# Kernel tuning notes

Hardware: AMD Instinct MI355X
Metric: run time of the kernel (lower is better)

The kernel has to match this reference:

```python
import jax, jax.numpy as jnp
import numpy as np

B, L, D, ORDER, POS, HID, LMAX = 4, 4096, 1024, 2, 65, 64, 4096
K2 = (POS - 1) // 2

def _layernorm(x, w, b, eps=1e-5):
    m = jnp.mean(x, -1, keepdims=True)
    v = jnp.mean((x - m) ** 2, -1, keepdims=True)
    return (x - m) * jax.lax.rsqrt(v + eps) * w + b

def _fftconv(x, h, d):
    # torch: rfft(h, 2L, norm='forward') * rfft(x, 2L) -> irfft(.., norm='forward')
    # net scaling equals standard (unnormalized fwd / 1-over-n inverse) circular conv,
    # which is exactly jnp.fft default conventions.
    n = 2 * x.shape[-1]
    y = jnp.fft.irfft(jnp.fft.rfft(x, n=n) * jnp.fft.rfft(h, n=n), n=n)[..., : x.shape[-1]]
    return y + x * d

def setup_inputs() -> dict:
    key = jax.random.key(0)
    ks = jax.random.split(key, 12)
    s = 0.05
    # PositionalEncoding buffers/params (deterministic init, as in torch __init__)
    t = np.linspace(0, 1, LMAX, dtype=np.float64)[:, None]
    t_pos = np.arange(LMAX, dtype=np.float64)[:, None]
    k = np.arange(K2, dtype=np.float64)[None, :]
    z = np.exp(1j * 2 * np.pi * k * t_pos / LMAX)
    pos_z = np.concatenate([t, z.real, z.imag], axis=-1).astype(np.float32)  # (LMAX, POS)
    pos_t = t.reshape(1, 1, LMAX).astype(np.float32)
    # ExponentialDecayWindow alphas (deterministic init)
    max_decay = np.log(0.01) / 0.3
    min_decay = np.log(0.01) / 1.5
    alphas = np.linspace(min_decay, max_decay, D).reshape(1, D, 1).astype(np.float32)
    H3 = (ORDER + 1) * D
    return dict(
        u=jax.random.normal(ks[0], (B, L, D), jnp.float32),
        norm1_w=jnp.ones((D,), jnp.float32), norm1_b=jnp.zeros((D,), jnp.float32),
        proj_w=jax.random.normal(ks[1], (H3, D), jnp.float32) * s,
        proj_b=jnp.zeros((H3,), jnp.float32),
        conv_w=jax.random.normal(ks[2], (H3, 1, 3), jnp.float32) * 0.3,
        conv_b=jnp.zeros((H3,), jnp.float32),
        pos_t=jnp.asarray(pos_t), pos_z=jnp.asarray(pos_z),
        fnn_w0=jax.random.normal(ks[3], (HID, POS), jnp.float32) * s,
        fnn_b0=jnp.zeros((HID,), jnp.float32),
        freq0=8.0 * jnp.ones((1, HID), jnp.float32),
        fnn_w1=jax.random.normal(ks[4], (HID, HID), jnp.float32) * s,
        fnn_b1=jnp.zeros((HID,), jnp.float32),
        freq1=8.0 * jnp.ones((1, HID), jnp.float32),
        fnn_w2=jax.random.normal(ks[5], (HID, HID), jnp.float32) * s,
        fnn_b2=jnp.zeros((HID,), jnp.float32),
        freq2=8.0 * jnp.ones((1, HID), jnp.float32),
        fnn_wout=jax.random.normal(ks[6], (ORDER * D, HID), jnp.float32) * s,
        alphas=jnp.asarray(alphas),
        hy_bias=jax.random.normal(ks[7], (ORDER, 1, D, 1), jnp.float32),
        norm2_w=jnp.ones((D,), jnp.float32), norm2_b=jnp.zeros((D,), jnp.float32),
        fc_w=jax.random.normal(ks[8], (D, D), jnp.float32) * s,
        fc_b=jnp.zeros((D,), jnp.float32),
    )

def reference(u, norm1_w, norm1_b, proj_w, proj_b, conv_w, conv_b, pos_t, pos_z,
              fnn_w0, fnn_b0, freq0, fnn_w1, fnn_b1, freq1, fnn_w2, fnn_b2, freq2,
              fnn_wout, alphas, hy_bias, norm2_w, norm2_b, fc_w, fc_b):
    Lq = u.shape[1]
    # Projection: LN -> Linear -> depthwise short conv (causal-ish, pad=2, slice :L)
    x = _layernorm(u, norm1_w, norm1_b)
    x = jnp.einsum('bld,hd->blh', x, proj_w) + proj_b          # (B,L,3D)
    x = x.transpose(0, 2, 1)                                   # (B,3D,L)
    x = jax.lax.conv_general_dilated(
        x, conv_w, window_strides=(1,), padding=[(2, 2)],
        feature_group_count=x.shape[1],
        dimension_numbers=('NCH', 'OIH', 'NCH'))[..., :Lq] + conv_b[None, :, None]
    # HyenaFilter: sin-MLP over positional features, then exp-decay window
    zf = pos_z[:Lq]                                            # (L,POS)
    h = jnp.sin(freq0 * (zf @ fnn_w0.T + fnn_b0))
    h = jnp.sin(freq1 * (h @ fnn_w1.T + fnn_b1))
    h = jnp.sin(freq2 * (h @ fnn_w2.T + fnn_b2))
    h = (h @ fnn_wout.T).T.reshape(ORDER, D, Lq)               # (order,D,L)
    decay = jnp.exp(alphas * pos_t[..., :Lq])                  # (1,D,L)
    h = h * decay
    # order-wise gated FFT long convolution (faithful to torch chunk/broadcast semantics)
    v = x[:, -1:, :]                                           # (B,1,L)
    for i in range(ORDER):
        v = x[:, i:i + 1, :] * _fftconv(v, h[i][None], hy_bias[i])  # (B,D,L)
    y = u + v.transpose(0, 2, 1)
    out = _layernorm(y, norm2_w, norm2_b) @ fc_w.T + fc_b      # activation = identity
    return out + y
```

## Files before the change

### kernel.cpp

```cpp
#include <hip/hip_runtime.h>
#include <hip/hip_bf16.h>

#define LL 4096
#define DD 1024
#define NB 4
#define N4 4096
#define KBINS 4097
#define NSLOT4 4366
#define PI_F 3.14159265358979323846f
#define INV4 (1.0f / 4096.0f)

typedef __attribute__((ext_vector_type(4))) float f32x4;
typedef __attribute__((ext_vector_type(8))) short s16x8;

#if defined(__has_builtin)
#if __has_builtin(__builtin_amdgcn_global_load_lds)
#define USE_GLOAD_LDS 1
#endif
#endif
#ifndef USE_GLOAD_LDS
#define USE_GLOAD_LDS 0
#endif

__device__ __forceinline__ unsigned short f2bf(float f) {
  unsigned int x = __float_as_uint(f);
  x += 0x7fffu + ((x >> 16) & 1u);
  return (unsigned short)(x >> 16);
}

__device__ __forceinline__ int SLT(int n) { return n + (n >> 4) + (n >> 8); }
__device__ __forceinline__ int brev12(int n) { return (int)(__brev((unsigned)n) >> 20); }

__device__ __forceinline__ float2 cmul(float2 a, float2 b) {
  return make_float2(a.x * b.x - a.y * b.y, a.x * b.y + a.y * b.x);
}
__device__ __forceinline__ float2 cadd(float2 a, float2 b) { return make_float2(a.x + b.x, a.y + b.y); }
__device__ __forceinline__ float2 csub(float2 a, float2 b) { return make_float2(a.x - b.x, a.y - b.y); }
__device__ __forceinline__ float2 conjf(float2 a) { return make_float2(a.x, -a.y); }
__device__ __forceinline__ float2 mulni(float2 v) { return make_float2(v.y, -v.x); }
__device__ __forceinline__ float2 mulpi(float2 v) { return make_float2(-v.y, v.x); }

template<bool INV>
__device__ __forceinline__ void bfly8(float2& A0, float2& A1, float2& A2, float2& A3,
                                      float2& A4, float2& A5, float2& A6, float2& A7,
                                      float2 w1, float2 w2, float2 w3) {
  const float C8 = 0.70710678118654752f;
  float2 t;
  t = cmul(w1, A1); float2 b0 = cadd(A0, t), b1 = csub(A0, t);
  t = cmul(w1, A3); float2 b2 = cadd(A2, t), b3 = csub(A2, t);
  t = cmul(w1, A5); float2 b4 = cadd(A4, t), b5 = csub(A4, t);
  t = cmul(w1, A7); float2 b6 = cadd(A6, t), b7 = csub(A6, t);
  t = cmul(w2, b2);                     float2 c0 = cadd(b0, t), c2 = csub(b0, t);
  t = cmul(w2, b3); t = INV ? mulpi(t) : mulni(t);
  float2 c1 = cadd(b1, t), c3 = csub(b1, t);
  t = cmul(w2, b6);                     float2 c4 = cadd(b4, t), c6 = csub(b4, t);
  t = cmul(w2, b7); t = INV ? mulpi(t) : mulni(t);
  float2 c5 = cadd(b5, t), c7 = csub(b5, t);
  t = cmul(w3, c4); A0 = cadd(c0, t); A4 = csub(c0, t);
  float2 e1 = cmul(w3, c5);
  t = INV ? make_float2(C8 * (e1.x - e1.y), C8 * (e1.y + e1.x))
          : make_float2(C8 * (e1.x + e1.y), C8 * (e1.y - e1.x));
  A1 = cadd(c1, t); A5 = csub(c1, t);
  float2 e2 = cmul(w3, c6); t = INV ? mulpi(e2) : mulni(e2);
  A2 = cadd(c2, t); A6 = csub(c2, t);
  float2 e3 = cmul(w3, c7);
  t = INV ? make_float2(-C8 * (e3.x + e3.y), C8 * (e3.x - e3.y))
          : make_float2(C8 * (e3.y - e3.x), -C8 * (e3.x + e3.y));
  A3 = cadd(c3, t); A7 = csub(c3, t);
}

template<bool INV>
__device__ __forceinline__ void fft4k_01(float2* Z, const float2* __restrict__ tw) {
  const int tid = threadIdx.x;
#pragma unroll
  for (int p = 0; p < 3; ++p) {
    const int hs = 3 * p;
    const int h = 1 << hs;
    const int j0 = tid & (h - 1);
    const int i = ((tid >> hs) << (hs + 3)) + j0;
    int s0 = SLT(i),         s1 = SLT(i + h),     s2 = SLT(i + 2 * h), s3 = SLT(i + 3 * h);
    int s4 = SLT(i + 4 * h), s5 = SLT(i + 5 * h), s6 = SLT(i + 6 * h), s7 = SLT(i + 7 * h);
    float2 a0 = Z[s0], a1 = Z[s1], a2 = Z[s2], a3 = Z[s3];
    float2 a4 = Z[s4], a5 = Z[s5], a6 = Z[s6], a7 = Z[s7];
    float2 w1 = tw[j0 << (12 - hs)];
    float2 w2 = tw[j0 << (11 - hs)];
    float2 w3 = tw[j0 << (10 - hs)];
    if (INV) { w1.y = -w1.y; w2.y = -w2.y; w3.y = -w3.y; }
    bfly8<INV>(a0, a1, a2, a3, a4, a5, a6, a7, w1, w2, w3);
    Z[s0] = a0; Z[s1] = a1; Z[s2] = a2; Z[s3] = a3;
    Z[s4] = a4; Z[s5] = a5; Z[s6] = a6; Z[s7] = a7;
    __builtin_amdgcn_wave_barrier();
  }
}

template<bool INV>
__device__ __forceinline__ void fft4k_p3(const float2* Z, const float2* __restrict__ tw,
                                         float2 d[8]) {
  const int t = threadIdx.x;
#pragma unroll
  for (int k = 0; k < 8; ++k) d[k] = Z[SLT(t + 512 * k)];
  float2 w1 = tw[t << 3], w2 = tw[t << 2], w3 = tw[t << 1];
  if (INV) { w1.y = -w1.y; w2.y = -w2.y; w3.y = -w3.y; }
  bfly8<INV>(d[0], d[1], d[2], d[3], d[4], d[5], d[6], d[7], w1, w2, w3);
}

__global__ void k_prep(float2* tw, const float* __restrict__ fcw,
                       unsigned short* __restrict__ fcwb) {
  const int bid = blockIdx.x;
  if (bid < 16) {
    int k = bid * 256 + threadIdx.x;
    float ang = -2.0f * PI_F * (float)k / 8192.0f;
    float s, c;
    sincosf(ang, &s, &c);
    tw[k] = make_float2(c, s);
  } else {
    int i = (bid - 16) * 256 + threadIdx.x;
    float4 v = ((const float4*)fcw)[i];
    ushort4 o;
    o.x = f2bf(v.x); o.y = f2bf(v.y); o.z = f2bf(v.z); o.w = f2bf(v.w);
    ((ushort4*)fcwb)[i] = o;
  }
}

__global__ __launch_bounds__(256) void k_lnproj_ffn(
    const float* __restrict__ u, const float* __restrict__ n1w, const float* __restrict__ n1b,
    const float* __restrict__ pw, const float* __restrict__ pb,
    float* __restrict__ xp0, float* __restrict__ xp1, float* __restrict__ xpL,
    const float* __restrict__ pos_z,
    const float* __restrict__ w0, const float* __restrict__ b0, const float* __restrict__ f0,
    const float* __restrict__ w1, const float* __restrict__ b1, const float* __restrict__ f1,
    const float* __restrict__ w2, const float* __restrict__ b2, const float* __restrict__ f2,
    float* __restrict__ hid2T) {
  __shared__ float zin[4][66];
  __shared__ float hbuf[4][64];
  const int g = threadIdx.x >> 6, lane = threadIdx.x & 63;
  if (blockIdx.x < (NB * LL) / 4) {
    const int r = blockIdx.x * 4 + g;
    const float* ur = u + (size_t)r * DD;
    float4 uv[4];
    float s = 0.f, sq = 0.f;
#pragma unroll
    for (int c = 0; c < 4; ++c) {
      uv[c] = ((const float4*)ur)[lane + 64 * c];
      s += uv[c].x + uv[c].y + uv[c].z + uv[c].w;
      sq += uv[c].x * uv[c].x + uv[c].y * uv[c].y + uv[c].z * uv[c].z + uv[c].w * uv[c].w;
    }
    for (int m = 1; m < 64; m <<= 1) { s += __shfl_xor(s, m); sq += __shfl_xor(sq, m); }
    const float mean = s * (1.0f / DD);
    const float var = sq * (1.0f / DD) - mean * mean;
    const float rs = rsqrtf(var + 1e-5f);
    float d0 = 0.f, d1 = 0.f, dL = 0.f;
    const float* pwL = pw + (size_t)3071 * DD;
#pragma unroll
    for (int c = 0; c < 4; ++c) {
      int i4 = lane + 64 * c;
      float4 wv = ((const float4*)n1w)[i4];
      float4 bv = ((const float4*)n1b)[i4];
      float4 p0 = ((const float4*)pw)[i4];
      float4 p1v = ((const float4*)(pw + DD))[i4];
      float4 pLv = ((const float4*)pwL)[i4];
      float xn;
      xn = (uv[c].x - mean) * rs * wv.x + bv.x; d0 += xn * p0.x; d1 += xn * p1v.x; dL += xn * pLv.x;
      xn = (uv[c].y - mean) * rs * wv.y + bv.y; d0 += xn * p0.y; d1 += xn * p1v.y; dL += xn * pLv.y;
      xn = (uv[c].z - mean) * rs * wv.z + bv.z; d0 += xn * p0.z; d1 += xn * p1v.z; dL += xn * pLv.z;
      xn = (uv[c].w - mean) * rs * wv.w + bv.w; d0 += xn * p0.w; d1 += xn * p1v.w; dL += xn * pLv.w;
    }
    for (int m = 1; m < 64; m <<= 1) {
      d0 += __shfl_xor(d0, m); d1 += __shfl_xor(d1, m); dL += __shfl_xor(dL, m);
    }
    if (lane == 0) {
      xp0[r] = d0 + pb[0];
      xp1[r] = d1 + pb[1];
      xpL[r] = dL + pb[3071];
    }
  } else {
    const int l0 = (blockIdx.x - (NB * LL) / 4) * 16;
    for (int it = 0; it < 4; ++it) {
      const int l = l0 + g * 4 + it;
      zin[g][lane] = pos_z[(size_t)l * 65 + lane];
      if (lane == 0) zin[g][64] = pos_z[(size_t)l * 65 + 64];
      __syncthreads();
      float acc = b0[lane];
#pragma unroll
      for (int k = 0; k < 65; ++k) acc += zin[g][k] * w0[lane * 65 + k];
      float hv = sinf(f0[lane] * acc);
      __syncthreads();
      hbuf[g][lane] = hv;
      __syncthreads();
      acc = b1[lane];
#pragma unroll
      for (int k = 0; k < 64; ++k) acc += hbuf[g][k] * w1[lane * 64 + k];
      hv = sinf(f1[lane] * acc);
      __syncthreads();
      hbuf[g][lane] = hv;
      __syncthreads();
      acc = b2[lane];
#pragma unroll
      for (int k = 0; k < 64; ++k) acc += hbuf[g][k] * w2[lane * 64 + k];
      hv = sinf(f2[lane] * acc);
      hid2T[(size_t)lane * LL + l] = hv;
      __syncthreads();
    }
  }
}

__global__ __launch_bounds__(256) void k_tapconv(
    const float* __restrict__ xp0, const float* __restrict__ xp1, const float* __restrict__ xpL,
    const float* __restrict__ cw, const float* __restrict__ cb,
    float* __restrict__ x0c, float* __restrict__ x1c, float* __restrict__ xLc) {
  int idx = blockIdx.x * 256 + threadIdx.x;
  if (idx >= NB * LL) return;
  int l = idx & (LL - 1);
  int base = idx - l;
  {
    const float* a = xp0 + base;
    float v = cw[2] * a[l];
    if (l >= 1) v += cw[1] * a[l - 1];
    if (l >= 2) v += cw[0] * a[l - 2];
    x0c[idx] = v + cb[0];
  }
  {
    const float* a = xp1 + base;
    float v = cw[5] * a[l];
    if (l >= 1) v += cw[4] * a[l - 1];
    if (l >= 2) v += cw[3] * a[l - 2];
    x1c[idx] = v + cb[1];
  }
  {
    const float* a = xpL + base;
    float v = cw[3071 * 3 + 2] * a[l];
    if (l >= 1) v += cw[3071 * 3 + 1] * a[l - 1];
    if (l >= 2) v += cw[3071 * 3 + 0] * a[l - 2];
    xLc[idx] = v + cb[3071];
  }
}

#define FG_CH 16
__global__ __launch_bounds__(256) void k_filter_gemm(
    const float* __restrict__ hid2T, const float* __restrict__ wout,
    const float* __restrict__ alphas, const float* __restrict__ pos_t,
    float* __restrict__ h) {
  __shared__ float wdl[FG_CH][64];
  const int cg = blockIdx.x & 127;
  const int lg = blockIdx.x >> 7;
  const int t = threadIdx.x;
  for (int idx = t; idx < FG_CH * 64; idx += 256) {
    int c = idx >> 6, k = idx & 63;
    wdl[c][k] = wout[(size_t)(cg * FG_CH + c) * 64 + k];
  }
  __syncthreads();
  const int l0 = lg * 1024 + 4 * t;
  float4 acc[FG_CH];
#pragma unroll
  for (int c = 0; c < FG_CH; ++c) acc[c] = make_float4(0.f, 0.f, 0.f, 0.f);
  for (int k = 0; k < 64; ++k) {
    float4 hv = *(const float4*)&hid2T[(size_t)k * LL + l0];
#pragma unroll
    for (int c = 0; c < FG_CH; ++c) {
      acc[c].x = fmaf(hv.x, wdl[c][k], acc[c].x);
      acc[c].y = fmaf(hv.y, wdl[c][k], acc[c].y);
      acc[c].z = fmaf(hv.z, wdl[c][k], acc[c].z);
      acc[c].w = fmaf(hv.w, wdl[c][k], acc[c].w);
    }
  }
  float4 tt = *(const float4*)&pos_t[l0];
#pragma unroll
  for (int c = 0; c < FG_CH; ++c) {
    int ch = cg * FG_CH + c;
    float a = alphas[ch & (DD - 1)];
    float4 o;
    o.x = acc[c].x * expf(a * tt.x);
    o.y = acc[c].y * expf(a * tt.y);
    o.z = acc[c].z * expf(a * tt.z);
    o.w = acc[c].w * expf(a * tt.w);
    *(float4*)&h[(size_t)ch * LL + l0] = o;
  }
}

__global__ __launch_bounds__(512, 4) void k_fft_filters(
    const float* __restrict__ h, const float* __restrict__ xLc,
    float2* __restrict__ Hs, float2* __restrict__ V0s, const float2* __restrict__ tw) {
  __shared__ float2 Z[NSLOT4];
  const int tid = threadIdx.x;
  const int bid = blockIdx.x;
  const float2* src = (bid < 2048) ? (const float2*)(h + (size_t)bid * LL)
                                   : (const float2*)(xLc + (size_t)(bid - 2048) * LL);
  float2* Out = (bid < 2048) ? (Hs + (size_t)bid * KBINS)
                             : (V0s + (size_t)(bid - 2048) * KBINS);
#pragma unroll
  for (int gi = 0; gi < 4; ++gi) {
    int j = tid + gi * 512;
    float2 v = src[j];
    int r = brev12(j);
    Z[SLT(r)] = v;
    Z[SLT(r + 1)] = make_float2(0.f, 0.f);
  }
  __syncthreads();
  fft4k_01<false>(Z, tw);
  __syncthreads();
  float2 dd[8];
  fft4k_p3<false>(Z, tw, dd);
#pragma unroll
  for (int k = 0; k < 8; ++k) Z[SLT(tid + 512 * k)] = dd[k];
  __syncthreads();
#pragma unroll
  for (int gi = 0; gi < 4; ++gi) {
    int k = tid + gi * 512;
    float2 zk = Z[SLT(k)];
    float2 zm = Z[SLT((N4 - k) & (N4 - 1))];
    float2 B = conjf(zm);
    float2 E = make_float2(0.5f * (zk.x + B.x), 0.5f * (zk.y + B.y));
    float2 F = make_float2(0.5f * (zk.x - B.x), 0.5f * (zk.y - B.y));
    float2 G = cmul(tw[k], F);
    float2 WO = mulni(G);
    Out[k] = cadd(E, WO);
    Out[N4 - k] = conjf(csub(E, WO));
  }
  if (tid == 0) {
    float2 zc = Z[SLT(2048)];
    float2 F = make_float2(0.f, zc.y);
    float2 G = cmul(tw[2048], F);
    Out[2048] = cadd(make_float2(zc.x, 0.f), mulni(G));
  }
}

__global__ __launch_bounds__(512, 4) void k_conv12(
    const float2* __restrict__ Hs, const float2* __restrict__ V0s,
    const float* __restrict__ x0c, const float* __restrict__ x1c, const float* __restrict__ xLc,
    const float* __restrict__ hyb, float* __restrict__ v2, const float2* __restrict__ tw) {
  __shared__ float2 Z[NSLOT4];
  const int b = blockIdx.x >> 10, d = blockIdx.x & 1023;
  const int tid = threadIdx.x;
  const float2* H0 = Hs + (size_t)d * KBINS;
  const float2* H1 = Hs + (size_t)(DD + d) * KBINS;
  const float2* V = V0s + (size_t)b * KBINS;
  const float2* g0 = (const float2*)(x0c + (size_t)b * LL);
  const float2* g1 = (const float2*)(x1c + (size_t)b * LL);
  const float2* v0 = (const float2*)(xLc + (size_t)b * LL);
  float2 gg0[4], vv0[4];
#pragma unroll
  for (int k = 0; k < 4; ++k) {
    int j = tid + 512 * k;
    gg0[k] = g0[j];
    vv0[k] = v0[j];
  }
#pragma unroll
  for (int gi = 0; gi < 4; ++gi) {
    int k = tid + gi * 512;
    int m = N4 - k;
    float2 Yk = cmul(V[k], H0[k]);
    float2 Ym = cmul(V[m], H0[m]);
    float2 B = conjf(Ym);
    float2 E = make_float2(0.5f * (Yk.x + B.x), 0.5f * (Yk.y + B.y));
    float2 F = make_float2(0.5f * (Yk.x - B.x), 0.5f * (Yk.y - B.y));
    float2 O = cmul(conjf(tw[k]), F);
    float2 iO = mulpi(O);
    Z[SLT(brev12(k))] = cadd(E, iO);
    if (k > 0) Z[SLT(brev12(m))] = conjf(csub(E, iO));
  }
  if (tid == 0) {
    float2 A = cmul(V[2048], H0[2048]);
    float2 F = make_float2(0.f, A.y);
    float2 O = cmul(conjf(tw[2048]), F);
    Z[SLT(brev12(2048))] = cadd(make_float2(A.x, 0.f), mulpi(O));
  }
  __syncthreads();
  fft4k_01<true>(Z, tw);
  __syncthreads();
  float2 dA[8];
  fft4k_p3<true>(Z, tw, dA);
  const float bd0 = hyb[d], bd1 = hyb[DD + d];
  float2 vsave[4];
#pragma unroll
  for (int k = 0; k < 4; ++k) {
    vsave[k] = make_float2(gg0[k].x * fmaf(dA[k].x, INV4, bd0 * vv0[k].x),
                           gg0[k].y * fmaf(dA[k].y, INV4, bd0 * vv0[k].y));
  }
  __syncthreads();
#pragma unroll
  for (int k = 0; k < 4; ++k) {
    int j = tid + 512 * k;
    int r = brev12(j);
    Z[SLT(r)] = vsave[k];
    Z[SLT(r + 1)] = make_float2(0.f, 0.f);
  }
  __syncthreads();
  fft4k_01<false>(Z, tw);
  __syncthreads();
  float2 dB[8];
  fft4k_p3<false>(Z, tw, dB);
#pragma unroll
  for (int k = 0; k < 8; ++k) Z[SLT(tid + 512 * k)] = dB[k];
  __syncthreads();
  float2 gg1[4];
#pragma unroll
  for (int k = 0; k < 4; ++k) gg1[k] = g1[tid + 512 * k];
  float2 zpk[4], zpm[4], z2048;
#pragma unroll
  for (int gi = 0; gi < 4; ++gi) {
    int k = tid + gi * 512;
    int m = N4 - k;
    float2 zk = Z[SLT(k)];
    float2 zm = Z[SLT(m & (N4 - 1))];
    float2 B = conjf(zm);
    float2 E = make_float2(0.5f * (zk.x + B.x), 0.5f * (zk.y + B.y));
    float2 F = make_float2(0.5f * (zk.x - B.x), 0.5f * (zk.y - B.y));
    float2 wk = tw[k];
    float2 G = cmul(wk, F);
    float2 WO = mulni(G);
    float2 Xk = cadd(E, WO);
    float2 Xm = conjf(csub(E, WO));
    float2 Yk = cmul(Xk, H1[k]);
    float2 Ym = cmul(Xm, H1[m]);
    float2 B2 = conjf(Ym);
    float2 E2 = make_float2(0.5f * (Yk.x + B2.x), 0.5f * (Yk.y + B2.y));
    float2 F2 = make_float2(0.5f * (Yk.x - B2.x), 0.5f * (Yk.y - B2.y));
    float2 O2 = cmul(conjf(wk), F2);
    float2 iO2 = mulpi(O2);
    zpk[gi] = cadd(E2, iO2);
    zpm[gi] = conjf(csub(E2, iO2));
  }
  if (tid == 0) {
    float2 zc = Z[SLT(2048)];
    float2 F = make_float2(0.f, zc.y);
    float2 G = cmul(tw[2048], F);
    float2 Xk = cadd(make_float2(zc.x, 0.f), mulni(G));
    float2 Y = cmul(Xk, H1[2048]);
    float2 F2 = make_float2(0.f, Y.y);
    float2 O2 = cmul(conjf(tw[2048]), F2);
    z2048 = cadd(make_float2(Y.x, 0.f), mulpi(O2));
  }
  __syncthreads();
#pragma unroll
  for (int gi = 0; gi < 4; ++gi) {
    int k = tid + gi * 512;
    Z[SLT(brev12(k))] = zpk[gi];
    if (k > 0) Z[SLT(brev12(N4 - k))] = zpm[gi];
  }
  if (tid == 0) Z[SLT(brev12(2048))] = z2048;
  __syncthreads();
  fft4k_01<true>(Z, tw);
  __syncthreads();
  float2 dC[8];
  fft4k_p3<true>(Z, tw, dC);
  float2* out2 = (float2*)(v2 + ((size_t)b * DD + d) * LL);
#pragma unroll
  for (int k = 0; k < 4; ++k) {
    int j = tid + 512 * k;
    out2[j] = make_float2(gg1[k].x * fmaf(dC[k].x, INV4, bd1 * vsave[k].x),
                          gg1[k].y * fmaf(dC[k].y, INV4, bd1 * vsave[k].y));
  }
}

__global__ __launch_bounds__(256) void k_transpose_add(const float* __restrict__ v2,
                                                       const float* __restrict__ u,
                                                       float* __restrict__ y) {
  __shared__ float T[64][65];
  const int bid = blockIdx.x;
  const int lt = bid & 63, dt = (bid >> 6) & 15, b = bid >> 10;
  const int t = threadIdx.x;
  const int tdr = t >> 2, lc0 = (t & 3) * 16;
  const float* vp = v2 + ((size_t)(b * DD + dt * 64 + tdr)) * LL + lt * 64 + lc0;
#pragma unroll
  for (int q = 0; q < 4; ++q) {
    float4 vv = ((const float4*)vp)[q];
    T[tdr][lc0 + 4 * q + 0] = vv.x;
    T[tdr][lc0 + 4 * q + 1] = vv.y;
    T[tdr][lc0 + 4 * q + 2] = vv.z;
    T[tdr][lc0 + 4 * q + 3] = vv.w;
  }
  __syncthreads();
  const int dc = t & 63, lg = t >> 6;
#pragma unroll
  for (int lr0 = 0; lr0 < 64; lr0 += 4) {
    int lr = lr0 + lg;
    size_t idx = ((size_t)b * LL + lt * 64 + lr) * DD + dt * 64 + dc;
    y[idx] = u[idx] + T[dc][lr];
  }
}

__global__ __launch_bounds__(256) void k_ln2(const float* __restrict__ y,
                                             const float* __restrict__ w,
                                             const float* __restrict__ bb,
                                             unsigned short* __restrict__ yln) {
  const int wid = threadIdx.x >> 6, lane = threadIdx.x & 63;
  const size_t r = (size_t)blockIdx.x * 4 + wid;
  const float* yr = y + r * DD;
  float4 v[4];
  float s = 0.f, sq = 0.f;
#pragma unroll
  for (int c = 0; c < 4; ++c) {
    v[c] = ((const float4*)yr)[lane + 64 * c];
    s += v[c].x + v[c].y + v[c].z + v[c].w;
    sq += v[c].x * v[c].x + v[c].y * v[c].y + v[c].z * v[c].z + v[c].w * v[c].w;
  }
  for (int m = 1; m < 64; m <<= 1) { s += __shfl_xor(s, m); sq += __shfl_xor(sq, m); }
  const float mean = s * (1.0f / DD);
  const float var = sq * (1.0f / DD) - mean * mean;
  const float rs = rsqrtf(var + 1e-5f);
#pragma unroll
  for (int c = 0; c < 4; ++c) {
    int i4 = lane + 64 * c;
    float4 wv = ((const float4*)w)[i4];
    float4 bv = ((const float4*)bb)[i4];
    ushort4 o;
    o.x = f2bf((v[c].x - mean) * rs * wv.x + bv.x);
    o.y = f2bf((v[c].y - mean) * rs * wv.y + bv.y);
    o.z = f2bf((v[c].z - mean) * rs * wv.z + bv.z);
    o.w = f2bf((v[c].w - mean) * rs * wv.w + bv.w);
    ((ushort4*)(yln + r * DD))[i4] = o;
  }
}

#define GBM 128
#define GBN 128
#define GBK 64
#if USE_GLOAD_LDS
#define LDK 64
#else
#define LDK 72
#endif

__global__ __launch_bounds__(256) void k_gemm(const short* __restrict__ A,
                                              const short* __restrict__ Bw,
                                              const float* __restrict__ fcb,
                                              const float* __restrict__ yy,
                                              float* __restrict__ out) {
  __shared__ short As[GBM * LDK];
  __shared__ short Bs[GBN * LDK];
  const int t = threadIdx.x;
  const int bm = blockIdx.x & 127;
  const int bn = blockIdx.x >> 7;
  const int wave = t >> 6, lane = t & 63;
  const int wr = wave >> 1, wc = wave & 1;
  const int rrow = lane & 15, kb = (lane >> 4) * 8;

  f32x4 acc[4][4];
#pragma unroll
  for (int i = 0; i < 4; ++i)
#pragma unroll
    for (int j = 0; j < 4; ++j) acc[i][j] = (f32x4){0.f, 0.f, 0.f, 0.f};

  const size_t abase = (size_t)(bm * GBM) * 1024;
  const size_t bbase = (size_t)(bn * GBN) * 1024;

  for (int k0 = 0; k0 < 1024; k0 += GBK) {
#if USE_GLOAD_LDS
    {
      const int r0 = wave * 32;
      const int lrow = lane >> 3, loff = (lane & 7) * 8;
#pragma unroll
      for (int q = 0; q < 4; ++q) {
        const int row = r0 + 8 * q + lrow;
        __builtin_amdgcn_global_load_lds(
            (const __attribute__((address_space(1))) void*)(A + abase + (size_t)row * 1024 + k0 + loff),
            (__attribute__((address_space(3))) void*)&As[(r0 + 8 * q) * LDK], 16, 0, 0);
        __builtin_amdgcn_global_load_lds(
            (const __attribute__((address_space(1))) void*)(Bw + bbase + (size_t)row * 1024 + k0 + loff),
            (__attribute__((address_space(3))) void*)&Bs[(r0 + 8 * q) * LDK], 16, 0, 0);
      }
    }
#else
#pragma unroll
    for (int c = 0; c < 4; ++c) {
      int chunk = c * 256 + t;
      int row = chunk >> 3, off = (chunk & 7) * 8;
      s16x8 av = *(const s16x8*)(A + abase + (size_t)row * 1024 + k0 + off);
      *(s16x8*)&As[row * LDK + off] = av;
      s16x8 bv = *(const s16x8*)(Bw + bbase + (size_t)row * 1024 + k0 + off);
      *(s16x8*)&Bs[row * LDK + off] = bv;
    }
#endif
    __syncthreads();
    s16x8 af[2][4], bfr[2][4];
#pragma unroll
    for (int ks = 0; ks < 2; ++ks) {
#pragma unroll
      for (int mr = 0; mr < 4; ++mr)
        af[ks][mr] = *(const s16x8*)&As[(wr * 64 + mr * 16 + rrow) * LDK + ks * 32 + kb];
#pragma unroll
      for (int nc = 0; nc < 4; ++nc)
        bfr[ks][nc] = *(const s16x8*)&Bs[(wc * 64 + nc * 16 + rrow) * LDK + ks * 32 + kb];
    }
#pragma unroll
    for (int ks = 0; ks < 2; ++ks)
#pragma unroll
      for (int mr = 0; mr < 4; ++mr)
#pragma unroll
        for (int nc = 0; nc < 4; ++nc)
          acc[mr][nc] = __builtin_amdgcn_mfma_f32_16x16x32_bf16(af[ks][mr], bfr[ks][nc],
                                                                acc[mr][nc], 0, 0, 0);
    __syncthreads();
  }
  const int cg = lane >> 4, cr = lane & 15;
#pragma unroll
  for (int mr = 0; mr < 4; ++mr)
#pragma unroll
    for (int nc = 0; nc < 4; ++nc) {
      f32x4 a = acc[mr][nc];
      int col = bn * GBN + wc * 64 + nc * 16 + cr;
#pragma unroll
      for (int q = 0; q < 4; ++q) {
        int row = bm * GBM + wr * 64 + mr * 16 + cg * 4 + q;
        size_t idx = (size_t)row * 1024 + col;
        out[idx] = a[q] + fcb[col] + yy[idx];
      }
    }
}

extern "C" void kernel_launch(void* const* d_in, const int* in_sizes, int n_in,
                              void* d_out, int out_size, void* d_ws, size_t ws_size,
                              hipStream_t stream) {
  const float* u      = (const float*)d_in[0];
  const float* n1w    = (const float*)d_in[1];
  const float* n1b    = (const float*)d_in[2];
  const float* projw  = (const float*)d_in[3];
  const float* projb  = (const float*)d_in[4];
  const float* convw  = (const float*)d_in[5];
  const float* convb  = (const float*)d_in[6];
  const float* pos_t  = (const float*)d_in[7];
  const float* pos_z  = (const float*)d_in[8];
  const float* w0     = (const float*)d_in[9];
  const float* b0     = (const float*)d_in[10];
  const float* f0     = (const float*)d_in[11];
  const float* w1     = (const float*)d_in[12];
  const float* b1     = (const float*)d_in[13];
  const float* f1     = (const float*)d_in[14];
  const float* w2     = (const float*)d_in[15];
  const float* b2     = (const float*)d_in[16];
  const float* f2     = (const float*)d_in[17];
  const float* wout   = (const float*)d_in[18];
  const float* alphas = (const float*)d_in[19];
  const float* hyb    = (const float*)d_in[20];
  const float* n2w    = (const float*)d_in[21];
  const float* n2b    = (const float*)d_in[22];
  const float* fcw    = (const float*)d_in[23];
  const float* fcb    = (const float*)d_in[24];

  char* wsb = (char*)d_ws;
  size_t off = 0;
  auto alloc = [&](size_t bytes) -> void* {
    off = (off + 255) & ~(size_t)255;
    void* p = wsb + off;
    off += bytes;
    return p;
  };
  float2* tw    = (float2*)alloc(sizeof(float2) * 4096);
  float*  xp0   = (float*)alloc(sizeof(float) * NB * LL);
  float*  xp1   = (float*)alloc(sizeof(float) * NB * LL);
  float*  xpL   = (float*)alloc(sizeof(float) * NB * LL);
  float*  x0c   = (float*)alloc(sizeof(float) * NB * LL);
  float*  x1c   = (float*)alloc(sizeof(float) * NB * LL);
  float*  xLc   = (float*)alloc(sizeof(float) * NB * LL);
  float*  hid2T = (float*)alloc(sizeof(float) * 64 * LL);
  float2* Hs    = (float2*)alloc(sizeof(float2) * 2 * DD * KBINS);
  float2* V0s   = (float2*)alloc(sizeof(float2) * NB * KBINS);
  float*  v2    = (float*)alloc(sizeof(float) * NB * DD * LL);
  unsigned short* fcwb = (unsigned short*)alloc(sizeof(unsigned short) * DD * DD);
  float*          y   = (float*)Hs;
  unsigned short* yln = (unsigned short*)v2;
  float*          h   = v2;
  (void)ws_size; (void)in_sizes; (void)n_in; (void)out_size;

  k_prep<<<16 + (DD * DD / 4) / 256, 256, 0, stream>>>(tw, fcw, fcwb);
  k_lnproj_ffn<<<(NB * LL) / 4 + LL / 16, 256, 0, stream>>>(
      u, n1w, n1b, projw, projb, xp0, xp1, xpL,
      pos_z, w0, b0, f0, w1, b1, f1, w2, b2, f2, hid2T);
  k_tapconv<<<(NB * LL) / 256, 256, 0, stream>>>(xp0, xp1, xpL, convw, convb, x0c, x1c, xLc);
  k_filter_gemm<<<512, 256, 0, stream>>>(hid2T, wout, alphas, pos_t, h);
  k_fft_filters<<<2048 + NB, 512, 0, stream>>>(h, xLc, Hs, V0s, tw);
  k_conv12<<<NB * DD, 512, 0, stream>>>(Hs, V0s, x0c, x1c, xLc, hyb, v2, tw);
  k_transpose_add<<<4096, 256, 0, stream>>>(v2, u, y);
  k_ln2<<<(NB * LL) / 4, 256, 0, stream>>>(y, n2w, n2b, yln);
  k_gemm<<<(16384 / GBM) * (1024 / GBN), 256, 0, stream>>>((const short*)yln, (const short*)fcwb,
                                                           fcb, y, (float*)d_out);
}
```

Measured before the change: 367.7 us.

## Process two FFT rows per block in filter and conv kernels

Each block of k_fft_filters and k_conv12 now handles two independent 4096-point FFT rows, interleaving their phases in two LDS buffers. The shared loads of the gate, V spectrum and input rows are also amortised across both channels. This halves the barrier count per row and adds independent work between syncs to hide latency. The cost is doubled LDS per block (about 70 KB) and more live registers, which lowers occupancy and may cause spills under launch_bounds(512,4).

Measured after the change: 382.8 us. 4.1% more time.

```diff
diff --git a/kernel.cpp b/kernel.cpp
--- a/kernel.cpp
+++ b/kernel.cpp
@@ -280,47 +280,60 @@
 __global__ __launch_bounds__(512, 4) void k_fft_filters(
     const float* __restrict__ h, const float* __restrict__ xLc,
     float2* __restrict__ Hs, float2* __restrict__ V0s, const float2* __restrict__ tw) {
-  __shared__ float2 Z[NSLOT4];
+  __shared__ float2 Z[2][NSLOT4];
   const int tid = threadIdx.x;
-  const int bid = blockIdx.x;
-  const float2* src = (bid < 2048) ? (const float2*)(h + (size_t)bid * LL)
-                                   : (const float2*)(xLc + (size_t)(bid - 2048) * LL);
-  float2* Out = (bid < 2048) ? (Hs + (size_t)bid * KBINS)
-                             : (V0s + (size_t)(bid - 2048) * KBINS);
-#pragma unroll
-  for (int gi = 0; gi < 4; ++gi) {
-    int j = tid + gi * 512;
-    float2 v = src[j];
-    int r = brev12(j);
-    Z[SLT(r)] = v;
-    Z[SLT(r + 1)] = make_float2(0.f, 0.f);
-  }
-  __syncthreads();
-  fft4k_01<false>(Z, tw);
-  __syncthreads();
-  float2 dd[8];
-  fft4k_p3<false>(Z, tw, dd);
-#pragma unroll
-  for (int k = 0; k < 8; ++k) Z[SLT(tid + 512 * k)] = dd[k];
-  __syncthreads();
-#pragma unroll
-  for (int gi = 0; gi < 4; ++gi) {
-    int k = tid + gi * 512;
-    float2 zk = Z[SLT(k)];
-    float2 zm = Z[SLT((N4 - k) & (N4 - 1))];
-    float2 B = conjf(zm);
-    float2 E = make_float2(0.5f * (zk.x + B.x), 0.5f * (zk.y + B.y));
-    float2 F = make_float2(0.5f * (zk.x - B.x), 0.5f * (zk.y - B.y));
-    float2 G = cmul(tw[k], F);
-    float2 WO = mulni(G);
-    Out[k] = cadd(E, WO);
-    Out[N4 - k] = conjf(csub(E, WO));
-  }
-  if (tid == 0) {
-    float2 zc = Z[SLT(2048)];
-    float2 F = make_float2(0.f, zc.y);
-    float2 G = cmul(tw[2048], F);
-    Out[2048] = cadd(make_float2(zc.x, 0.f), mulni(G));
+#pragma unroll
+  for (int c = 0; c < 2; ++c) {
+    const int row = 2 * blockIdx.x + c;
+    const float2* src = (row < 2048) ? (const float2*)(h + (size_t)row * LL)
+                                     : (const float2*)(xLc + (size_t)(row - 2048) * LL);
+    float2* Zc = Z[c];
+#pragma unroll
+    for (int gi = 0; gi < 4; ++gi) {
+      int j = tid + gi * 512;
+      float2 v = src[j];
+      int r = brev12(j);
+      Zc[SLT(r)] = v;
+      Zc[SLT(r + 1)] = make_float2(0.f, 0.f);
+    }
+  }
+  __syncthreads();
+#pragma unroll
+  for (int c = 0; c < 2; ++c) fft4k_01<false>(Z[c], tw);
+  __syncthreads();
+#pragma unroll
+  for (int c = 0; c < 2; ++c) {
+    float2 dd[8];
+    fft4k_p3<false>(Z[c], tw, dd);
+#pragma unroll
+    for (int k = 0; k < 8; ++k) Z[c][SLT(tid + 512 * k)] = dd[k];
+  }
+  __syncthreads();
+#pragma unroll
+  for (int c = 0; c < 2; ++c) {
+    const int row = 2 * blockIdx.x + c;
+    float2* Out = (row < 2048) ? (Hs + (size_t)row * KBINS)
+                               : (V0s + (size_t)(row - 2048) * KBINS);
+    float2* Zc = Z[c];
+#pragma unroll
+    for (int gi = 0; gi < 4; ++gi) {
+      int k = tid + gi * 512;
+      float2 zk = Zc[SLT(k)];
+      float2 zm = Zc[SLT((N4 - k) & (N4 - 1))];
+      float2 B = conjf(zm);
+      float2 E = make_float2(0.5f * (zk.x + B.x), 0.5f * (zk.y + B.y));
+      float2 F = make_float2(0.5f * (zk.x - B.x), 0.5f * (zk.y - B.y));
+      float2 G = cmul(tw[k], F);
+      float2 WO = mulni(G);
+      Out[k] = cadd(E, WO);
+      Out[N4 - k] = conjf(csub(E, WO));
+    }
+    if (tid == 0) {
+      float2 zc = Zc[SLT(2048)];
+      float2 F = make_float2(0.f, zc.y);
+      float2 G = cmul(tw[2048], F);
+      Out[2048] = cadd(make_float2(zc.x, 0.f), mulni(G));
+    }
   }
 }
 
@@ -328,127 +341,157 @@
     const float2* __restrict__ Hs, const float2* __restrict__ V0s,
     const float* __restrict__ x0c, const float* __restrict__ x1c, const float* __restrict__ xLc,
     const float* __restrict__ hyb, float* __restrict__ v2, const float2* __restrict__ tw) {
-  __shared__ float2 Z[NSLOT4];
-  const int b = blockIdx.x >> 10, d = blockIdx.x & 1023;
+  __shared__ float2 Z[2][NSLOT4];
+  const int b = blockIdx.x >> 9, dp = blockIdx.x & 511;
   const int tid = threadIdx.x;
-  const float2* H0 = Hs + (size_t)d * KBINS;
-  const float2* H1 = Hs + (size_t)(DD + d) * KBINS;
   const float2* V = V0s + (size_t)b * KBINS;
+#pragma unroll
+  for (int c = 0; c < 2; ++c) {
+    const int d = 2 * dp + c;
+    const float2* H0 = Hs + (size_t)d * KBINS;
+    float2* Zc = Z[c];
+#pragma unroll
+    for (int gi = 0; gi < 4; ++gi) {
+      int k = tid + gi * 512;
+      int m = N4 - k;
+      float2 Yk = cmul(V[k], H0[k]);
+      float2 Ym = cmul(V[m], H0[m]);
+      float2 B = conjf(Ym);
+      float2 E = make_float2(0.5f * (Yk.x + B.x), 0.5f * (Yk.y + B.y));
+      float2 F = make_float2(0.5f * (Yk.x - B.x), 0.5f * (Yk.y - B.y));
+      float2 O = cmul(conjf(tw[k]), F);
+      float2 iO = mulpi(O);
+      Zc[SLT(brev12(k))] = cadd(E, iO);
+      if (k > 0) Zc[SLT(brev12(m))] = conjf(csub(E, iO));
+    }
+    if (tid == 0) {
+      float2 A = cmul(V[2048], H0[2048]);
+      float2 F = make_float2(0.f, A.y);
+      float2 O = cmul(conjf(tw[2048]), F);
+      Zc[SLT(brev12(2048))] = cadd(make_float2(A.x, 0.f), mulpi(O));
+    }
+  }
+  __syncthreads();
+#pragma unroll
+  for (int c = 0; c < 2; ++c) fft4k_01<true>(Z[c], tw);
+  __syncthreads();
   const float2* g0 = (const float2*)(x0c + (size_t)b * LL);
   const float2* g1 = (const float2*)(x1c + (size_t)b * LL);
   const float2* v0 = (const float2*)(xLc + (size_t)b * LL);
-  float2 gg0[4], vv0[4];
+  float2 gg[4], vv[4];
 #pragma unroll
   for (int k = 0; k < 4; ++k) {
     int j = tid + 512 * k;
-    gg0[k] = g0[j];
-    vv0[k] = v0[j];
-  }
-#pragma unroll
-  for (int gi = 0; gi < 4; ++gi) {
-    int k = tid + gi * 512;
-    int m = N4 - k;
-    float2 Yk = cmul(V[k], H0[k]);
-    float2 Ym = cmul(V[m], H0[m]);
-    float2 B = conjf(Ym);
-    float2 E = make_float2(0.5f * (Yk.x + B.x), 0.5f * (Yk.y + B.y));
-    float2 F = make_float2(0.5f * (Yk.x - B.x), 0.5f * (Yk.y - B.y));
-    float2 O = cmul(conjf(tw[k]), F);
-    float2 iO = mulpi(O);
-    Z[SLT(brev12(k))] = cadd(E, iO);
-    if (k > 0) Z[SLT(brev12(m))] = conjf(csub(E, iO));
-  }
-  if (tid == 0) {
-    float2 A = cmul(V[2048], H0[2048]);
-    float2 F = make_float2(0.f, A.y);
-    float2 O = cmul(conjf(tw[2048]), F);
-    Z[SLT(brev12(2048))] = cadd(make_float2(A.x, 0.f), mulpi(O));
-  }
-  __syncthreads();
-  fft4k_01<true>(Z, tw);
-  __syncthreads();
-  float2 dA[8];
-  fft4k_p3<true>(Z, tw, dA);
-  const float bd0 = hyb[d], bd1 = hyb[DD + d];
-  float2 vsave[4];
-#pragma unroll
-  for (int k = 0; k < 4; ++k) {
-    vsave[k] = make_float2(gg0[k].x * fmaf(dA[k].x, INV4, bd0 * vv0[k].x),
-                           gg0[k].y * fmaf(dA[k].y, INV4, bd0 * vv0[k].y));
-  }
-  __syncthreads();
-#pragma unroll
-  for (int k = 0; k < 4; ++k) {
-    int j = tid + 512 * k;
-    int r = brev12(j);
-    Z[SLT(r)] = vsave[k];
-    Z[SLT(r + 1)] = make_float2(0.f, 0.f);
-  }
-  __syncthreads();
-  fft4k_01<false>(Z, tw);
-  __syncthreads();
-  float2 dB[8];
-  fft4k_p3<false>(Z, tw, dB);
-#pragma unroll
-  for (int k = 0; k < 8; ++k) Z[SLT(tid + 512 * k)] = dB[k];
+    gg[k] = g0[j];
+    vv[k] = v0[j];
+  }
+  float2 vsave[2][4];
+#pragma unroll
+  for (int c = 0; c < 2; ++c) {
+    float2 dA[8];
+    fft4k_p3<true>(Z[c], tw, dA);
+    const float bd0 = hyb[2 * dp + c];
+#pragma unroll
+    for (int k = 0; k < 4; ++k) {
+      vsave[c][k] = make_float2(gg[k].x * fmaf(dA[k].x, INV4, bd0 * vv[k].x),
+                                gg[k].y * fmaf(dA[k].y, INV4, bd0 * vv[k].y));
+    }
+  }
+  __syncthreads();
+#pragma unroll
+  for (int c = 0; c < 2; ++c) {
+    float2* Zc = Z[c];
+#pragma unroll
+    for (int k = 0; k < 4; ++k) {
+      int j = tid + 512 * k;
+      int r = brev12(j);
+      Zc[SLT(r)] = vsave[c][k];
+      Zc[SLT(r + 1)] = make_float2(0.f, 0.f);
+    }
+  }
+  __syncthreads();
+#pragma unroll
+  for (int c = 0; c < 2; ++c) fft4k_01<false>(Z[c], tw);
+  __syncthreads();
+#pragma unroll
+  for (int c = 0; c < 2; ++c) {
+    float2 dB[8];
+    fft4k_p3<false>(Z[c], tw, dB);
+#pragma unroll
+    for (int k = 0; k < 8; ++k) Z[c][SLT(tid + 512 * k)] = dB[k];
+  }
+  __syncthreads();
+  float2 zpk[2][4], zpm[2][4], z2048[2];
+#pragma unroll
+  for (int c = 0; c < 2; ++c) {
+    const float2* H1 = Hs + (size_t)(DD + 2 * dp + c) * KBINS;
+    float2* Zc = Z[c];
+#pragma unroll
+    for (int gi = 0; gi < 4; ++gi) {
+      int k = tid + gi * 512;
+      int m = N4 - k;
+      float2 zk = Zc[SLT(k)];
+      float2 zm = Zc[SLT(m & (N4 - 1))];
+      float2 B = conjf(zm);
+      float2 E = make_float2(0.5f * (zk.x + B.x), 0.5f * (zk.y + B.y));
+      float2 F = make_float2(0.5f * (zk.x - B.x), 0.5f * (zk.y - B.y));
+      float2 wk = tw[k];
+      float2 G = cmul(wk, F);
+      float2 WO = mulni(G);
+      float2 Xk = cadd(E, WO);
+      float2 Xm = conjf(csub(E, WO));
+      float2 Yk = cmul(Xk, H1[k]);
+      float2 Ym = cmul(Xm, H1[m]);
+      float2 B2 = conjf(Ym);
+      float2 E2 = make_float2(0.5f * (Yk.x + B2.x), 0.5f * (Yk.y + B2.y));
+      float2 F2 = make_float2(0.5f * (Yk.x - B2.x), 0.5f * (Yk.y - B2.y));
+      float2 O2 = cmul(conjf(wk), F2);
+      float2 iO2 = mulpi(O2);
+      zpk[c][gi] = cadd(E2, iO2);
+      zpm[c][gi] = conjf(csub(E2, iO2));
+    }
+    if (tid == 0) {
+      float2 zc = Zc[SLT(2048)];
+      float2 F = make_float2(0.f, zc.y);
+      float2 G = cmul(tw[2048], F);
+      float2 Xk = cadd(make_float2(zc.x, 0.f), mulni(G));
+      float2 Y = cmul(Xk, H1[2048]);
+      float2 F2 = make_float2(0.f, Y.y);
+      float2 O2 = cmul(conjf(tw[2048]), F2);
+      z2048[c] = cadd(make_float2(Y.x, 0.f), mulpi(O2));
+    }
+  }
+  __syncthreads();
+#pragma unroll
+  for (int c = 0; c < 2; ++c) {
+    float2* Zc = Z[c];
+#pragma unroll
+    for (int gi = 0; gi < 4; ++gi) {
+      int k = tid + gi * 512;
+      Zc[SLT(brev12(k))] = zpk[c][gi];
+      if (k > 0) Zc[SLT(brev12(N4 - k))] = zpm[c][gi];
+    }
+    if (tid == 0) Zc[SLT(brev12(2048))] = z2048[c];
+  }
+  __syncthreads();
+#pragma unroll
+  for (int c = 0; c < 2; ++c) fft4k_01<true>(Z[c], tw);
   __syncthreads();
   float2 gg1[4];
 #pragma unroll
   for (int k = 0; k < 4; ++k) gg1[k] = g1[tid + 512 * k];
-  float2 zpk[4], zpm[4], z2048;
-#pragma unroll
-  for (int gi = 0; gi < 4; ++gi) {
-    int k = tid + gi * 512;
-    int m = N4 - k;
-    float2 zk = Z[SLT(k)];
-    float2 zm = Z[SLT(m & (N4 - 1))];
-    float2 B = conjf(zm);
-    float2 E = make_float2(0.5f * (zk.x + B.x), 0.5f * (zk.y + B.y));
-    float2 F = make_float2(0.5f * (zk.x - B.x), 0.5f * (zk.y - B.y));
-    float2 wk = tw[k];
-    float2 G = cmul(wk, F);
-    float2 WO = mulni(G);
-    float2 Xk = cadd(E, WO);
-    float2 Xm = conjf(csub(E, WO));
-    float2 Yk = cmul(Xk, H1[k]);
-    float2 Ym = cmul(Xm, H1[m]);
-    float2 B2 = conjf(Ym);
-    float2 E2 = make_float2(0.5f * (Yk.x + B2.x), 0.5f * (Yk.y + B2.y));
-    float2 F2 = make_float2(0.5f * (Yk.x - B2.x), 0.5f * (Yk.y - B2.y));
-    float2 O2 = cmul(conjf(wk), F2);
-    float2 iO2 = mulpi(O2);
-    zpk[gi] = cadd(E2, iO2);
-    zpm[gi] = conjf(csub(E2, iO2));
-  }
-  if (tid == 0) {
-    float2 zc = Z[SLT(2048)];
-    float2 F = make_float2(0.f, zc.y);
-    float2 G = cmul(tw[2048], F);
-    float2 Xk = cadd(make_float2(zc.x, 0.f), mulni(G));
-    float2 Y = cmul(Xk, H1[2048]);
-    float2 F2 = make_float2(0.f, Y.y);
-    float2 O2 = cmul(conjf(tw[2048]), F2);
-    z2048 = cadd(make_float2(Y.x, 0.f), mulpi(O2));
-  }
-  __syncthreads();
-#pragma unroll
-  for (int gi = 0; gi < 4; ++gi) {
-    int k = tid + gi * 512;
-    Z[SLT(brev12(k))] = zpk[gi];
-    if (k > 0) Z[SLT(brev12(N4 - k))] = zpm[gi];
-  }
-  if (tid == 0) Z[SLT(brev12(2048))] = z2048;
-  __syncthreads();
-  fft4k_01<true>(Z, tw);
-  __syncthreads();
-  float2 dC[8];
-  fft4k_p3<true>(Z, tw, dC);
-  float2* out2 = (float2*)(v2 + ((size_t)b * DD + d) * LL);
-#pragma unroll
-  for (int k = 0; k < 4; ++k) {
-    int j = tid + 512 * k;
-    out2[j] = make_float2(gg1[k].x * fmaf(dC[k].x, INV4, bd1 * vsave[k].x),
-                          gg1[k].y * fmaf(dC[k].y, INV4, bd1 * vsave[k].y));
+#pragma unroll
+  for (int c = 0; c < 2; ++c) {
+    float2 dC[8];
+    fft4k_p3<true>(Z[c], tw, dC);
+    const float bd1 = hyb[DD + 2 * dp + c];
+    float2* out2 = (float2*)(v2 + ((size_t)b * DD + 2 * dp + c) * LL);
+#pragma unroll
+    for (int k = 0; k < 4; ++k) {
+      int j = tid + 512 * k;
+      out2[j] = make_float2(gg1[k].x * fmaf(dC[k].x, INV4, bd1 * vsave[c][k].x),
+                            gg1[k].y * fmaf(dC[k].y, INV4, bd1 * vsave[c][k].y));
+    }
   }
 }
 
@@ -668,8 +711,8 @@
       pos_z, w0, b0, f0, w1, b1, f1, w2, b2, f2, hid2T);
   k_tapconv<<<(NB * LL) / 256, 256, 0, stream>>>(xp0, xp1, xpL, convw, convb, x0c, x1c, xLc);
   k_filter_gemm<<<512, 256, 0, stream>>>(hid2T, wout, alphas, pos_t, h);
-  k_fft_filters<<<2048 + NB, 512, 0, stream>>>(h, xLc, Hs, V0s, tw);
-  k_conv12<<<NB * DD, 512, 0, stream>>>(Hs, V0s, x0c, x1c, xLc, hyb, v2, tw);
+  k_fft_filters<<<(2048 + NB) / 2, 512, 0, stream>>>(h, xLc, Hs, V0s, tw);
+  k_conv12<<<NB * DD / 2, 512, 0, stream>>>(Hs, V0s, x0c, x1c, xLc, hyb, v2, tw);
   k_transpose_add<<<4096, 256, 0, stream>>>(v2, u, y);
   k_ln2<<<(NB * LL) / 4, 256, 0, stream>>>(y, n2w, n2b, yln);
   k_gemm<<<(16384 / GBM) * (1024 / GBN), 256, 0, stream>>>((const short*)yln, (const short*)fcwb,
```
